# Kernel optimization log

Hardware: AMD Instinct MI355X
Metric: run time of the kernel (lower is better)

## Reference

```python
import jax, jax.numpy as jnp
import numpy as np

N = 50000        # nodes per node type (user, item)
D_IN = 256       # node_in_dim
D_REL = 64       # rel_in_dim
K = 8            # num_heads
D_OUT = 32       # node_out_dim (per head); K*D_OUT = 256
D_RELOUT = 32    # rel_out_dim (per head)
E = 300000       # edges per relation direction
SLOPE = 0.2

# relations: 0 = user-rates->item, 1 = item-rated-by->user,
#            2 = user-clicks->item, 3 = item-clicked-by->user
STYPE = [0, 1, 0, 1]   # 0=user, 1=item
DTYPE = [1, 0, 1, 0]
REV   = [1, 0, 3, 2]
GROUP = [[0, 2], [1, 3], [0, 2], [1, 3]]  # relations sharing this relation's dtype


def setup_inputs() -> dict:
    key = jax.random.key(0)
    ks = jax.random.split(key, 16)
    feats = jax.random.normal(ks[0], (4, N, D_IN), jnp.float32)
    rel_feats = jax.random.normal(ks[1], (4, D_REL), jnp.float32)
    src_rates = jax.random.randint(ks[2], (E,), 0, N, jnp.int32)
    dst_rates = jax.random.randint(ks[3], (E,), 0, N, jnp.int32)
    src_clicks = jax.random.randint(ks[4], (E,), 0, N, jnp.int32)
    dst_clicks = jax.random.randint(ks[5], (E,), 0, N, jnp.int32)
    s = 0.05
    W_node = s * jax.random.normal(ks[6], (2, D_IN, K * D_OUT), jnp.float32)          # fc_node per ntype (no bias)
    Wr = s * jax.random.normal(ks[7], (4, D_REL, 2 * K * D_OUT), jnp.float32)         # fc_rel per etype (no bias)
    Wres = s * jax.random.normal(ks[8], (2, D_IN, K * D_OUT), jnp.float32)            # fc_res per ntype
    bres = s * jax.random.normal(ks[9], (2, K * D_OUT), jnp.float32)
    resw = jax.random.uniform(ks[10], (2,), jnp.float32)                              # res_weight per ntype
    rel_attn = s * jax.random.normal(ks[11], (4, K, D_OUT), jnp.float32)              # rel_attn per etype
    Wupd = s * jax.random.normal(ks[12], (4, D_REL, K * D_RELOUT), jnp.float32)       # fc_upd per etype
    bupd = s * jax.random.normal(ks[13], (4, K * D_RELOUT), jnp.float32)
    return dict(feats=feats, rel_feats=rel_feats, src_rates=src_rates, dst_rates=dst_rates,
                src_clicks=src_clicks, dst_clicks=dst_clicks, W_node=W_node, Wr=Wr,
                Wres=Wres, bres=bres, resw=resw, rel_attn=rel_attn, Wupd=Wupd, bupd=bupd)


def _leaky(x):
    return jnp.where(x >= 0, x, SLOPE * x)


def _rel_graph_conv(hs, hd, attn, src, dst):
    """GAT-style conv for one relation. hs,hd: (N,K,D_OUT); attn: (K,2*D_OUT)."""
    el = (hs * attn[:, :D_OUT]).sum(-1)                    # (N_src, K)
    er = (hd * attn[:, D_OUT:]).sum(-1)                    # (N_dst, K)
    e = _leaky(el[src] + er[dst])                          # (E, K)
    # edge softmax grouped by destination node
    m = jax.ops.segment_max(e, dst, num_segments=N)        # (N, K)
    m = jnp.where(jnp.isfinite(m), m, 0.0)                 # nodes with no incoming edges
    ex = jnp.exp(e - m[dst])
    z = jax.ops.segment_sum(ex, dst, num_segments=N)
    a = ex / z[dst]                                        # (E, K)
    msg = hs[src] * a[:, :, None]                          # (E, K, D_OUT)
    out = jax.ops.segment_sum(msg, dst, num_segments=N)    # (N, K, D_OUT)
    return jax.nn.relu(out.reshape(N, K * D_OUT))


def reference(feats, rel_feats, src_rates, dst_rates, src_clicks, dst_clicks,
              W_node, Wr, Wres, bres, resw, rel_attn, Wupd, bupd):
    srcs = [src_rates, dst_rates, src_clicks, dst_clicks]
    dsts = [dst_rates, src_rates, dst_clicks, src_clicks]

    node_rel = []
    for r in range(4):
        # feat_src = feats of stype nodes (stored under the reverse relation); feat_dst under r
        hs = (feats[REV[r]] @ W_node[STYPE[r]]).reshape(N, K, D_OUT)
        hd = (feats[r] @ W_node[DTYPE[r]]).reshape(N, K, D_OUT)
        attn = (rel_feats[r] @ Wr[r]).reshape(K, 2 * D_OUT)
        conv = _rel_graph_conv(hs, hd, attn, srcs[r], dsts[r])
        # residual per destination node type
        alpha = jax.nn.sigmoid(resw[DTYPE[r]])
        inherit = feats[r] @ Wres[DTYPE[r]] + bres[DTYPE[r]]
        node_rel.append(alpha * conv + (1.0 - alpha) * inherit)

    # cross-relation attention per relation (over relations sharing the same dtype)
    out_feats = []
    for r in range(4):
        h = jnp.stack([node_rel[i] for i in GROUP[r]], 0).reshape(len(GROUP[r]), N, K, D_OUT)
        scores = (rel_attn[r] * h).sum(-1, keepdims=True)           # (R, N, K, 1)
        w = jax.nn.softmax(_leaky(scores), axis=0)
        out_feats.append((w * h).sum(0).reshape(N, K * D_OUT))
    out_nodes = jnp.stack(out_feats, 0)                             # (4, N, K*D_OUT)

    rel_out = jnp.einsum('rd,rdo->ro', rel_feats, Wupd) + bupd      # (4, K*D_RELOUT)
    return out_nodes, rel_out
```

## Files before the change

kernel.cpp:

```cpp
#include <hip/hip_runtime.h>

typedef unsigned short u16;
typedef __bf16 bf16x8 __attribute__((ext_vector_type(8)));
typedef float f32x4 __attribute__((ext_vector_type(4)));

#define N_NODES 50000
#define N_EDGES 300000
#define NP      12800000
#define NE8     400000

#define WP_OFF    0L
#define ATTN_OFF  524288L
#define ALPHA_OFF 532480L
#define P_OFF     532544L
#define EL_OFF    102932544L
#define ER_OFF    109332544L
#define CNT_OFF   115732544L
#define CUR_OFF   116532544L
#define ROW_OFF   117332544L
#define BS_OFF    118132560L
#define COL_OFF   118135696L

__device__ __forceinline__ float bf2f(u16 u){
  union { unsigned int i; float f; } v; v.i = ((unsigned int)u) << 16; return v.f;
}
__device__ __forceinline__ u16 f2bf(float f){
  union { float f; unsigned int i; } v; v.f = f;
  unsigned int x = v.i;
  x += 0x7fffu + ((x >> 16) & 1u);
  return (u16)(x >> 16);
}
__device__ __forceinline__ float leaky(float x){ return x >= 0.f ? x : 0.2f * x; }

__global__ void small_k(const float* __restrict__ rel_feats, const float* __restrict__ Wr,
                        const float* __restrict__ Wupd, const float* __restrict__ bupd,
                        const float* __restrict__ resw,
                        float* __restrict__ attn, float* __restrict__ alpha,
                        float* __restrict__ out_tail){
  int r = blockIdx.x, t = threadIdx.x;
  for (int j = t; j < 512; j += 256){
    float s = 0.f;
    for (int d = 0; d < 64; ++d)
      s += rel_feats[r*64 + d] * Wr[(r*64 + d)*512 + j];
    attn[r*512 + j] = s;
  }
  {
    float s = 0.f;
    for (int d = 0; d < 64; ++d)
      s += rel_feats[r*64 + d] * Wupd[(r*64 + d)*256 + t];
    out_tail[r*256 + t] = s + bupd[r*256 + t];
  }
  if (r == 0 && t < 2) alpha[t] = 1.f / (1.f + __expf(-resw[t]));
}

__global__ void prepack_k(const float* __restrict__ Wn, const float* __restrict__ Wres,
                          u16* __restrict__ Wp){
  int tid = blockIdx.x*256 + threadIdx.x;
  int m = tid >> 16, rem = tid & 65535;
  int kt = rem >> 13, rem2 = rem & 8191;
  int n = rem2 >> 5, kk = rem2 & 31;
  const float* src = (m < 2) ? (Wn + m*65536) : (Wres + (m - 2)*65536);
  Wp[tid] = f2bf(src[(kt*32 + kk)*256 + n]);
}

__global__ __launch_bounds__(256) void gemm_k(const float* __restrict__ A,
                                              const u16* __restrict__ Wpn, const u16* __restrict__ Wpr,
                                              const float* __restrict__ bias,
                                              const float* __restrict__ alpha_ws, int tix,
                                              u16* __restrict__ Pout, float* __restrict__ out,
                                              const float* __restrict__ attnL, const float* __restrict__ attnR,
                                              float* __restrict__ ELb, float* __restrict__ ERb){
  __shared__ __align__(16) u16 Btn[256*40];
  __shared__ __align__(16) u16 Btr[256*40];
  const int tid = threadIdx.x;
  const int lane = tid & 63, wave = tid >> 6;
  const int quad = lane >> 4, n0 = lane & 15;
  const int wrow = blockIdx.x*64 + wave*16;
  const int ar = wrow + n0;
  f32x4 accn[16], accr[16];
#pragma unroll
  for (int i = 0; i < 16; ++i){ accn[i] = f32x4{0.f,0.f,0.f,0.f}; accr[i] = f32x4{0.f,0.f,0.f,0.f}; }

  for (int kt = 0; kt < 8; ++kt){
    __syncthreads();
#pragma unroll
    for (int c = 0; c < 4; ++c){
      int ci = tid + c*256;
      int nn = ci >> 2, gg = ci & 3;
      *(uint4*)(Btn + nn*40 + gg*8) = *(const uint4*)(Wpn + kt*8192 + nn*32 + gg*8);
      *(uint4*)(Btr + nn*40 + gg*8) = *(const uint4*)(Wpr + kt*8192 + nn*32 + gg*8);
    }
    __syncthreads();
    union { bf16x8 v; u16 s[8]; } af;
    if (ar < N_NODES){
      const float* ap = A + (size_t)ar*256 + kt*32 + quad*8;
      f32x4 a0 = *(const f32x4*)ap;
      f32x4 a1 = *(const f32x4*)(ap + 4);
#pragma unroll
      for (int j = 0; j < 4; ++j){ af.s[j] = f2bf(a0[j]); af.s[4+j] = f2bf(a1[j]); }
    } else {
#pragma unroll
      for (int j = 0; j < 8; ++j) af.s[j] = 0;
    }
#pragma unroll
    for (int nt = 0; nt < 16; ++nt){
      bf16x8 bn = *(const bf16x8*)(Btn + (nt*16 + n0)*40 + quad*8);
      bf16x8 br = *(const bf16x8*)(Btr + (nt*16 + n0)*40 + quad*8);
      accn[nt] = __builtin_amdgcn_mfma_f32_16x16x32_bf16(af.v, bn, accn[nt], 0, 0, 0);
      accr[nt] = __builtin_amdgcn_mfma_f32_16x16x32_bf16(af.v, br, accr[nt], 0, 0, 0);
    }
  }
  const float one_m_al = 1.f - alpha_ws[tix];
#pragma unroll
  for (int nt = 0; nt < 16; ++nt){
    int col = nt*16 + n0;
    float b = bias[col];
#pragma unroll
    for (int reg = 0; reg < 4; ++reg){
      int row = wrow + quad*4 + reg;
      if (row < N_NODES){
        out[(size_t)row*256 + col] = one_m_al * (accr[nt][reg] + b);
        Pout[(size_t)row*256 + col] = f2bf(accn[nt][reg]);
      }
    }
  }
  float selL[4] = {0.f, 0.f, 0.f, 0.f};
  float selR[4] = {0.f, 0.f, 0.f, 0.f};
#pragma unroll
  for (int k = 0; k < 8; ++k){
    float a0 = attnL[k*64 + n0],      a1 = attnL[k*64 + 16 + n0];
    float b0 = attnR[k*64 + n0],      b1 = attnR[k*64 + 16 + n0];
#pragma unroll
    for (int reg = 0; reg < 4; ++reg){
      float ev = accn[2*k][reg]*a0 + accn[2*k+1][reg]*a1;
      float rv = accn[2*k][reg]*b0 + accn[2*k+1][reg]*b1;
      ev += __shfl_xor(ev, 1); ev += __shfl_xor(ev, 2);
      ev += __shfl_xor(ev, 4); ev += __shfl_xor(ev, 8);
      rv += __shfl_xor(rv, 1); rv += __shfl_xor(rv, 2);
      rv += __shfl_xor(rv, 4); rv += __shfl_xor(rv, 8);
      if (n0 == k)     selL[reg] = ev;
      if (n0 == 8 + k) selR[reg] = rv;
    }
  }
#pragma unroll
  for (int reg = 0; reg < 4; ++reg){
    int row = wrow + quad*4 + reg;
    if (row < N_NODES){
      if (n0 < 8) ELb[row*8 + n0]       = selL[reg];
      else        ERb[row*8 + (n0 - 8)] = selR[reg];
    }
  }
}

__global__ void zero_k(int* __restrict__ p, int n){
  int i = blockIdx.x*256 + threadIdx.x; if (i < n) p[i] = 0;
}
__global__ void hist_k(const int* __restrict__ sr, const int* __restrict__ dr,
                       const int* __restrict__ sc, const int* __restrict__ dc,
                       int* __restrict__ counts){
  int r = blockIdx.y; int e = blockIdx.x*256 + threadIdx.x;
  if (e >= N_EDGES) return;
  const int* dst = (r == 0) ? dr : (r == 1) ? sr : (r == 2) ? dc : sc;
  atomicAdd(&counts[r*N_NODES + dst[e]], 1);
}
__global__ void scan1_k(const int* __restrict__ counts, int* __restrict__ rowptr,
                        int* __restrict__ bsums){
  int r = blockIdx.y; int i = blockIdx.x*256 + threadIdx.x;
  int lane = threadIdx.x & 63, wave = threadIdx.x >> 6;
  int v = (i < N_NODES) ? counts[r*N_NODES + i] : 0;
  int orig = v;
  for (int off = 1; off < 64; off <<= 1){ int t = __shfl_up(v, off); if (lane >= off) v += t; }
  __shared__ int wsum[4];
  if (lane == 63) wsum[wave] = v;
  __syncthreads();
  int add = 0;
  for (int w = 0; w < wave; ++w) add += wsum[w];
  v += add;
  if (i < N_NODES) rowptr[r*(N_NODES+1) + i] = v - orig;
  if (threadIdx.x == 255) bsums[r*196 + blockIdx.x] = v;
}
__global__ void scan2_k(int* __restrict__ bsums){
  int lane = threadIdx.x & 63, r = threadIdx.x >> 6;
  int carry = 0;
  for (int c = 0; c < 4; ++c){
    int i = c*64 + lane;
    int v = (i < 196) ? bsums[r*196 + i] : 0;
    int orig = v;
    for (int off = 1; off < 64; off <<= 1){ int t = __shfl_up(v, off); if (lane >= off) v += t; }
    int excl = v - orig + carry;
    if (i < 196) bsums[r*196 + i] = excl;
    carry += __shfl(v, 63);
  }
}
__global__ void scan3_k(const int* __restrict__ bsums, int* __restrict__ rowptr){
  int r = blockIdx.y; int i = blockIdx.x*256 + threadIdx.x;
  if (i < N_NODES) rowptr[r*(N_NODES+1) + i] += bsums[r*196 + blockIdx.x];
  if (i == N_NODES) rowptr[r*(N_NODES+1) + N_NODES] = N_EDGES;
}
__global__ void scatter_k(const int* __restrict__ sr, const int* __restrict__ dr,
                          const int* __restrict__ sc, const int* __restrict__ dc,
                          const int* __restrict__ rowptr, int* __restrict__ cur,
                          int* __restrict__ colsrc){
  int r = blockIdx.y; int e = blockIdx.x*256 + threadIdx.x;
  if (e >= N_EDGES) return;
  const int* dst = (r == 0) ? dr : (r == 1) ? sr : (r == 2) ? dc : sc;
  const int* src = (r == 0) ? sr : (r == 1) ? dr : (r == 2) ? sc : dc;
  int d = dst[e];
  int pos = rowptr[r*(N_NODES+1) + d] + atomicAdd(&cur[r*N_NODES + d], 1);
  colsrc[r*N_EDGES + pos] = src[e];
}

__global__ __launch_bounds__(256) void aggcross_k(
    const int* __restrict__ rowptr, const int* __restrict__ colsrc,
    const float* __restrict__ EL, const float* __restrict__ ER,
    const u16* __restrict__ P, const float* __restrict__ rel_attn,
    const float* __restrict__ alpha_ws, float* __restrict__ out){
  const int g = blockIdx.y;
  const int wave = threadIdx.x >> 6, lane = threadIdx.x & 63;
  const int n = blockIdx.x*4 + wave;
  if (n >= N_NODES) return;
  const int k0 = lane >> 3, j = lane & 7;
  const float al = alpha_ws[g ^ 1];
  f32x4 h[2];
#pragma unroll
  for (int which = 0; which < 2; ++which){
    const int r = g + which*2;
    const int rp0 = rowptr[r*(N_NODES+1) + n], rp1 = rowptr[r*(N_NODES+1) + n + 1];
    const float er = ER[(size_t)r*NE8 + n*8 + k0];
    const float* el = EL + (size_t)r*NE8;
    const int* cs = colsrc + r*N_EDGES;
    const u16* Ps = P + (size_t)(r ^ 1)*NP;

    float z = 0.f, a0 = 0.f, a1 = 0.f, a2 = 0.f, a3 = 0.f;
    for (int base = rp0; base < rp1; base += 8){
      const int cnt = rp1 - base;
      const int m = cnt < 8 ? cnt : 8;
      int sj = cs[base + (j < m ? j : 0)];
      float x = leaky(el[sj*8 + k0] + er);
      float p = (j < m) ? __expf(x - 10.f) : 0.f;
      ushort4 hv[8]; float pv[8];
#pragma unroll
      for (int t = 0; t < 8; ++t){
        if (t < m){
          int s = __shfl(sj, t);
          hv[t] = *(const ushort4*)(Ps + (size_t)s*256 + lane*4);
          pv[t] = __shfl(p, (lane & 56) | t);
        }
      }
#pragma unroll
      for (int t = 0; t < 8; ++t){
        if (t < m){
          float q = pv[t];
          z += q;
          a0 += q*bf2f(hv[t].x); a1 += q*bf2f(hv[t].y);
          a2 += q*bf2f(hv[t].z); a3 += q*bf2f(hv[t].w);
        }
      }
    }
    float inv = (rp1 > rp0) ? 1.f / z : 0.f;
    f32x4 inh = *(const f32x4*)(out + (size_t)r*NP + (size_t)n*256 + lane*4);
    h[which][0] = al * fmaxf(a0*inv, 0.f) + inh[0];
    h[which][1] = al * fmaxf(a1*inv, 0.f) + inh[1];
    h[which][2] = al * fmaxf(a2*inv, 0.f) + inh[2];
    h[which][3] = al * fmaxf(a3*inv, 0.f) + inh[3];
  }
#pragma unroll
  for (int which = 0; which < 2; ++which){
    int rr = g + which*2;
    const float* ra = rel_attn + rr*256 + k0*32 + j*4;
    float s0 = 0.f, s1 = 0.f;
#pragma unroll
    for (int jj = 0; jj < 4; ++jj){
      float a = ra[jj];
      s0 += a * h[0][jj]; s1 += a * h[1][jj];
    }
    s0 += __shfl_xor(s0, 1); s1 += __shfl_xor(s1, 1);
    s0 += __shfl_xor(s0, 2); s1 += __shfl_xor(s1, 2);
    s0 += __shfl_xor(s0, 4); s1 += __shfl_xor(s1, 4);
    float l0 = leaky(s0), l1 = leaky(s1);
    float mx = fmaxf(l0, l1);
    float e0 = __expf(l0 - mx), e1 = __expf(l1 - mx);
    float w0 = e0 / (e0 + e1), w1 = 1.f - w0;
    f32x4 o;
#pragma unroll
    for (int jj = 0; jj < 4; ++jj) o[jj] = w0*h[0][jj] + w1*h[1][jj];
    *(f32x4*)(out + ((size_t)rr*N_NODES + n)*256 + lane*4) = o;
  }
}

extern "C" void kernel_launch(void* const* d_in, const int* in_sizes, int n_in,
                              void* d_out, int out_size, void* d_ws, size_t ws_size,
                              hipStream_t stream) {
  (void)in_sizes; (void)n_in; (void)out_size; (void)ws_size;
  const float* feats      = (const float*)d_in[0];
  const float* rel_feats  = (const float*)d_in[1];
  const int*   src_rates  = (const int*)d_in[2];
  const int*   dst_rates  = (const int*)d_in[3];
  const int*   src_clicks = (const int*)d_in[4];
  const int*   dst_clicks = (const int*)d_in[5];
  const float* W_node     = (const float*)d_in[6];
  const float* Wr         = (const float*)d_in[7];
  const float* Wres       = (const float*)d_in[8];
  const float* bres       = (const float*)d_in[9];
  const float* resw       = (const float*)d_in[10];
  const float* rel_attn   = (const float*)d_in[11];
  const float* Wupd       = (const float*)d_in[12];
  const float* bupd       = (const float*)d_in[13];

  char* w = (char*)d_ws;
  u16*   Wp     = (u16*)(w + WP_OFF);
  float* attn   = (float*)(w + ATTN_OFF);
  float* alpha  = (float*)(w + ALPHA_OFF);
  u16*   P      = (u16*)(w + P_OFF);
  float* EL     = (float*)(w + EL_OFF);
  float* ER     = (float*)(w + ER_OFF);
  int*   counts = (int*)(w + CNT_OFF);
  int*   cur    = (int*)(w + CUR_OFF);
  int*   rowptr = (int*)(w + ROW_OFF);
  int*   bsums  = (int*)(w + BS_OFF);
  int*   colsrc = (int*)(w + COL_OFF);
  float* out    = (float*)d_out;

  static const int DT[4] = {1, 0, 1, 0};

  zero_k<<<1563, 256, 0, stream>>>(counts, 400000);
  small_k<<<4, 256, 0, stream>>>(rel_feats, Wr, Wupd, bupd, resw, attn, alpha,
                                 out + (size_t)4*NP);
  prepack_k<<<1024, 256, 0, stream>>>(W_node, Wres, Wp);

  hist_k<<<dim3(1172, 4), 256, 0, stream>>>(src_rates, dst_rates, src_clicks, dst_clicks, counts);
  scan1_k<<<dim3(196, 4), 256, 0, stream>>>(counts, rowptr, bsums);
  scan2_k<<<1, 256, 0, stream>>>(bsums);
  scan3_k<<<dim3(196, 4), 256, 0, stream>>>(bsums, rowptr);
  scatter_k<<<dim3(1172, 4), 256, 0, stream>>>(src_rates, dst_rates, src_clicks, dst_clicks,
                                               rowptr, cur, colsrc);

  for (int i = 0; i < 4; ++i)
    gemm_k<<<782, 256, 0, stream>>>(feats + (size_t)i*NP,
                                    Wp + DT[i]*65536, Wp + (2 + DT[i])*65536,
                                    bres + DT[i]*256, alpha, DT[i],
                                    P + (size_t)i*NP, out + (size_t)i*NP,
                                    attn + (i ^ 1)*512, attn + i*512 + 32,
                                    EL + (size_t)(i ^ 1)*NE8, ER + (size_t)i*NE8);

  aggcross_k<<<dim3(12500, 2), 256, 0, stream>>>(rowptr, colsrc, EL, ER, P,
                                                 rel_attn, alpha, out);
}
```

Before: 1.033 ms.

## Retile node GEMM so each wave owns 64 columns, dropping LDS staging

```diff
diff --git a/kernel.cpp b/kernel.cpp
--- a/kernel.cpp
+++ b/kernel.cpp
@@ -63,91 +63,101 @@
   Wp[tid] = f2bf(src[(kt*32 + kk)*256 + n]);
 }
 
-__global__ __launch_bounds__(256) void gemm_k(const float* __restrict__ A,
+__global__ __launch_bounds__(256, 2) void gemm_k(const float* __restrict__ A,
                                               const u16* __restrict__ Wpn, const u16* __restrict__ Wpr,
                                               const float* __restrict__ bias,
                                               const float* __restrict__ alpha_ws, int tix,
                                               u16* __restrict__ Pout, float* __restrict__ out,
                                               const float* __restrict__ attnL, const float* __restrict__ attnR,
                                               float* __restrict__ ELb, float* __restrict__ ERb){
-  __shared__ __align__(16) u16 Btn[256*40];
-  __shared__ __align__(16) u16 Btr[256*40];
   const int tid = threadIdx.x;
   const int lane = tid & 63, wave = tid >> 6;
   const int quad = lane >> 4, n0 = lane & 15;
-  const int wrow = blockIdx.x*64 + wave*16;
-  const int ar = wrow + n0;
-  f32x4 accn[16], accr[16];
-#pragma unroll
-  for (int i = 0; i < 16; ++i){ accn[i] = f32x4{0.f,0.f,0.f,0.f}; accr[i] = f32x4{0.f,0.f,0.f,0.f}; }
+  const int wrow = blockIdx.x*64;
+  const int cbase = wave*64;
+  f32x4 accn[4][4], accr[4][4];
+#pragma unroll
+  for (int f = 0; f < 4; ++f)
+#pragma unroll
+    for (int nt = 0; nt < 4; ++nt){
+      accn[f][nt] = f32x4{0.f,0.f,0.f,0.f};
+      accr[f][nt] = f32x4{0.f,0.f,0.f,0.f};
+    }
 
   for (int kt = 0; kt < 8; ++kt){
-    __syncthreads();
-#pragma unroll
-    for (int c = 0; c < 4; ++c){
-      int ci = tid + c*256;
-      int nn = ci >> 2, gg = ci & 3;
-      *(uint4*)(Btn + nn*40 + gg*8) = *(const uint4*)(Wpn + kt*8192 + nn*32 + gg*8);
-      *(uint4*)(Btr + nn*40 + gg*8) = *(const uint4*)(Wpr + kt*8192 + nn*32 + gg*8);
-    }
-    __syncthreads();
-    union { bf16x8 v; u16 s[8]; } af;
-    if (ar < N_NODES){
-      const float* ap = A + (size_t)ar*256 + kt*32 + quad*8;
-      f32x4 a0 = *(const f32x4*)ap;
-      f32x4 a1 = *(const f32x4*)(ap + 4);
-#pragma unroll
-      for (int j = 0; j < 4; ++j){ af.s[j] = f2bf(a0[j]); af.s[4+j] = f2bf(a1[j]); }
-    } else {
-#pragma unroll
-      for (int j = 0; j < 8; ++j) af.s[j] = 0;
-    }
-#pragma unroll
-    for (int nt = 0; nt < 16; ++nt){
-      bf16x8 bn = *(const bf16x8*)(Btn + (nt*16 + n0)*40 + quad*8);
-      bf16x8 br = *(const bf16x8*)(Btr + (nt*16 + n0)*40 + quad*8);
-      accn[nt] = __builtin_amdgcn_mfma_f32_16x16x32_bf16(af.v, bn, accn[nt], 0, 0, 0);
-      accr[nt] = __builtin_amdgcn_mfma_f32_16x16x32_bf16(af.v, br, accr[nt], 0, 0, 0);
-    }
-  }
+    const u16* bpn = Wpn + kt*8192 + (cbase + n0)*32 + quad*8;
+    const u16* bpr = Wpr + kt*8192 + (cbase + n0)*32 + quad*8;
+    bf16x8 bn[4], br[4];
+#pragma unroll
+    for (int nt = 0; nt < 4; ++nt){
+      bn[nt] = *(const bf16x8*)(bpn + nt*16*32);
+      br[nt] = *(const bf16x8*)(bpr + nt*16*32);
+    }
+    union { bf16x8 v; u16 s[8]; } af[4];
+#pragma unroll
+    for (int f = 0; f < 4; ++f){
+      int row = wrow + f*16 + n0;
+      if (row < N_NODES){
+        const float* ap = A + (size_t)row*256 + kt*32 + quad*8;
+        f32x4 a0 = *(const f32x4*)ap;
+        f32x4 a1 = *(const f32x4*)(ap + 4);
+#pragma unroll
+        for (int j = 0; j < 4; ++j){ af[f].s[j] = f2bf(a0[j]); af[f].s[4+j] = f2bf(a1[j]); }
+      } else {
+#pragma unroll
+        for (int j = 0; j < 8; ++j) af[f].s[j] = 0;
+      }
+    }
+#pragma unroll
+    for (int f = 0; f < 4; ++f)
+#pragma unroll
+      for (int nt = 0; nt < 4; ++nt){
+        accn[f][nt] = __builtin_amdgcn_mfma_f32_16x16x32_bf16(af[f].v, bn[nt], accn[f][nt], 0, 0, 0);
+        accr[f][nt] = __builtin_amdgcn_mfma_f32_16x16x32_bf16(af[f].v, br[nt], accr[f][nt], 0, 0, 0);
+      }
+  }
+
   const float one_m_al = 1.f - alpha_ws[tix];
 #pragma unroll
-  for (int nt = 0; nt < 16; ++nt){
-    int col = nt*16 + n0;
-    float b = bias[col];
+  for (int f = 0; f < 4; ++f)
+#pragma unroll
+    for (int nt = 0; nt < 4; ++nt){
+      int col = cbase + nt*16 + n0;
+      float b = bias[col];
+#pragma unroll
+      for (int reg = 0; reg < 4; ++reg){
+        int row = wrow + f*16 + quad*4 + reg;
+        if (row < N_NODES){
+          out[(size_t)row*256 + col] = one_m_al * (accr[f][nt][reg] + b);
+          Pout[(size_t)row*256 + col] = f2bf(accn[f][nt][reg]);
+        }
+      }
+    }
+
+  const int h0 = 2*wave, h1 = 2*wave + 1;
+  const float aL00 = attnL[h0*64 + n0], aL01 = attnL[h0*64 + 16 + n0];
+  const float aL10 = attnL[h1*64 + n0], aL11 = attnL[h1*64 + 16 + n0];
+  const float aR00 = attnR[h0*64 + n0], aR01 = attnR[h0*64 + 16 + n0];
+  const float aR10 = attnR[h1*64 + n0], aR11 = attnR[h1*64 + 16 + n0];
+#pragma unroll
+  for (int f = 0; f < 4; ++f){
 #pragma unroll
     for (int reg = 0; reg < 4; ++reg){
-      int row = wrow + quad*4 + reg;
+      float e0 = accn[f][0][reg]*aL00 + accn[f][1][reg]*aL01;
+      float e1 = accn[f][2][reg]*aL10 + accn[f][3][reg]*aL11;
+      float r0 = accn[f][0][reg]*aR00 + accn[f][1][reg]*aR01;
+      float r1 = accn[f][2][reg]*aR10 + accn[f][3][reg]*aR11;
+      e0 += __shfl_xor(e0, 1); e0 += __shfl_xor(e0, 2); e0 += __shfl_xor(e0, 4); e0 += __shfl_xor(e0, 8);
+      e1 += __shfl_xor(e1, 1); e1 += __shfl_xor(e1, 2); e1 += __shfl_xor(e1, 4); e1 += __shfl_xor(e1, 8);
+      r0 += __shfl_xor(r0, 1); r0 += __shfl_xor(r0, 2); r0 += __shfl_xor(r0, 4); r0 += __shfl_xor(r0, 8);
+      r1 += __shfl_xor(r1, 1); r1 += __shfl_xor(r1, 2); r1 += __shfl_xor(r1, 4); r1 += __shfl_xor(r1, 8);
+      int row = wrow + f*16 + quad*4 + reg;
       if (row < N_NODES){
-        out[(size_t)row*256 + col] = one_m_al * (accr[nt][reg] + b);
-        Pout[(size_t)row*256 + col] = f2bf(accn[nt][reg]);
-      }
-    }
-  }
-  float selL[4] = {0.f, 0.f, 0.f, 0.f};
-  float selR[4] = {0.f, 0.f, 0.f, 0.f};
-#pragma unroll
-  for (int k = 0; k < 8; ++k){
-    float a0 = attnL[k*64 + n0],      a1 = attnL[k*64 + 16 + n0];
-    float b0 = attnR[k*64 + n0],      b1 = attnR[k*64 + 16 + n0];
-#pragma unroll
-    for (int reg = 0; reg < 4; ++reg){
-      float ev = accn[2*k][reg]*a0 + accn[2*k+1][reg]*a1;
-      float rv = accn[2*k][reg]*b0 + accn[2*k+1][reg]*b1;
-      ev += __shfl_xor(ev, 1); ev += __shfl_xor(ev, 2);
-      ev += __shfl_xor(ev, 4); ev += __shfl_xor(ev, 8);
-      rv += __shfl_xor(rv, 1); rv += __shfl_xor(rv, 2);
-      rv += __shfl_xor(rv, 4); rv += __shfl_xor(rv, 8);
-      if (n0 == k)     selL[reg] = ev;
-      if (n0 == 8 + k) selR[reg] = rv;
-    }
-  }
-#pragma unroll
-  for (int reg = 0; reg < 4; ++reg){
-    int row = wrow + quad*4 + reg;
-    if (row < N_NODES){
-      if (n0 < 8) ELb[row*8 + n0]       = selL[reg];
-      else        ERb[row*8 + (n0 - 8)] = selR[reg];
+        if (n0 == 0)      ELb[row*8 + h0] = e0;
+        else if (n0 == 1) ELb[row*8 + h1] = e1;
+        else if (n0 == 2) ERb[row*8 + h0] = r0;
+        else if (n0 == 3) ERb[row*8 + h1] = r1;
+      }
     }
   }
 }
```

New measurement: 927.0 us. -10.3%, faster.
